# Performance work log

Hardware: AMD Instinct MI355X
Metric: run time of the kernel (lower is better)

## Reference

```python
import jax, jax.numpy as jnp
import numpy as np

BN, C, T = 512, 32, 4096
TARGET = 256


def setup_inputs() -> dict:
    key = jax.random.key(0)
    k1, k2, k3 = jax.random.split(key, 3)
    features = jax.random.normal(k1, (BN, C, T), dtype=jnp.float32)
    mask = jax.random.uniform(k2, (BN, C, T), dtype=jnp.float32)
    valid_lengths = jax.random.randint(k3, (BN,), 0, T, dtype=jnp.int64)
    return {"features": features, "mask": mask,
            "valid_lengths": valid_lengths, "target_len": TARGET}


def _pool(v, si, ei, counts):
    # v: [BN, C, T]; si/ei: [BN, K]; counts: [BN, K]
    bn, c, t = v.shape
    cs = jnp.cumsum(v, axis=-1)
    cs = jnp.concatenate([jnp.zeros((bn, c, 1), cs.dtype), cs], axis=-1)  # [BN,C,T+1]
    s = jnp.take_along_axis(cs, si[:, None, :], axis=-1)  # [BN,C,K] (idx broadcast over C)
    e = jnp.take_along_axis(cs, ei[:, None, :], axis=-1)
    return (e - s) / counts[:, None, :].astype(v.dtype)


def reference(features, mask, valid_lengths, target_len):
    bn, c, t = features.shape
    K = max(int(target_len), 1)
    lengths = jnp.clip(valid_lengths, 1, t)                       # [BN]
    # zero out everything before the trailing valid window
    time_idx = jnp.arange(t, dtype=lengths.dtype)
    rmask = (time_idx[None, :] >= (t - lengths)[:, None]).astype(features.dtype)  # [BN,T]
    f = features * rmask[:, None, :]
    m = mask * rmask[:, None, :]
    # adaptive-pool bin boundaries within the trailing window
    offsets = (t - lengths)[:, None]                              # [BN,1]
    steps = jnp.arange(K + 1, dtype=lengths.dtype)                # [K+1]
    scaled = lengths[:, None] * steps[None, :]                    # [BN,K+1]
    start_rel = scaled[:, :-1] // K
    end_rel = (scaled[:, 1:] + K - 1) // K
    si = jnp.clip(start_rel + offsets, 0, t)
    ei = jnp.clip(end_rel + offsets, 0, t)
    counts = jnp.clip(ei - si, 1, None)                           # [BN,K]
    pooled_feats = _pool(f, si, ei, counts)
    pooled_mask = _pool(m, si, ei, counts)
    return pooled_feats, pooled_mask
```

## Files before the change

### kernel.cpp

```cpp
#include <hip/hip_runtime.h>

#define BN 512
#define CCH 32
#define TT 4096

__device__ __forceinline__ int padidx(int i) { return i + ((i >> 5) << 2); }

__global__ __launch_bounds__(256) void adaptive_pool_lds(
    const float* __restrict__ f, const float* __restrict__ m,
    const int* __restrict__ vlen,
    float* __restrict__ out_f, float* __restrict__ out_m, int K)
{
    __shared__ float sf[4608];
    __shared__ float sm[4608];

    int bc = blockIdx.x;
    int b  = bc / CCH;

    bool is64 = ((vlen[1] | vlen[3] | vlen[5] | vlen[7] |
                  vlen[9] | vlen[11] | vlen[13] | vlen[15]) == 0);
    int len = is64 ? vlen[2 * b] : vlen[b];

    int L = len < 1 ? 1 : (len > TT ? TT : len);
    int off = TT - L;
    int a0 = off & ~3;

    const float* fr = f + (size_t)bc * TT;
    const float* mr = m + (size_t)bc * TT;

    int nv = (TT - a0) >> 2;
    for (int idx = threadIdx.x; idx < nv; idx += 256) {
        int t0 = a0 + (idx << 2);
        float4 vf = *(const float4*)(fr + t0);
        float4 vm = *(const float4*)(mr + t0);
        int p = padidx(t0);
        *(float4*)(&sf[p]) = vf;
        *(float4*)(&sm[p]) = vm;
    }
    __syncthreads();

    for (int k = threadIdx.x; k < K; k += 256) {
        unsigned uL = (unsigned)L, uK = (unsigned)K, uk = (unsigned)k;
        int si = off + (int)((uL * uk) / uK);
        int ei = off + (int)((uL * (uk + 1u) + uK - 1u) / uK);
        if (ei > TT) ei = TT;
        int count = ei - si;
        if (count < 1) count = 1;

        float af = 0.0f, am = 0.0f;
        for (int t = si; t < ei; ++t) {
            int p = padidx(t);
            af += sf[p];
            am += sm[p];
        }
        float inv = 1.0f / (float)count;
        size_t o = (size_t)bc * K + k;
        out_f[o] = af * inv;
        out_m[o] = am * inv;
    }
}

extern "C" void kernel_launch(void* const* d_in, const int* in_sizes, int n_in,
                              void* d_out, int out_size, void* d_ws, size_t ws_size,
                              hipStream_t stream) {
    const float* f    = (const float*)d_in[0];
    const float* m    = (const float*)d_in[1];
    const int*   vlen = (const int*)d_in[2];

    int K = out_size / (2 * BN * CCH);
    if (K < 1) K = 1;

    float* out_f = (float*)d_out;
    float* out_m = out_f + (size_t)BN * CCH * K;

    int grid = BN * CCH;
    adaptive_pool_lds<<<grid, 256, 0, stream>>>(f, m, vlen, out_f, out_m, K);
}
```

Before: 61.60 us.

## Process multiple rows per block with register-prefetched software pipelining

Each block now handles eight (batch,channel) rows in a grid-strided fashion. The global loads for the next row are issued into registers before pooling the current row from LDS, so memory latency overlaps with compute. The grid shrinks eightfold, which cuts block launch overhead but risks tail imbalance across rows with varying valid lengths and higher register pressure.

```diff
diff --git a/kernel.cpp b/kernel.cpp
--- a/kernel.cpp
+++ b/kernel.cpp
@@ -3,10 +3,11 @@
 #define BN 512
 #define CCH 32
 #define TT 4096
+#define RPB 8
 
 __device__ __forceinline__ int padidx(int i) { return i + ((i >> 5) << 2); }
 
-__global__ __launch_bounds__(256) void adaptive_pool_lds(
+__global__ __launch_bounds__(256) void pool_pipe(
     const float* __restrict__ f, const float* __restrict__ m,
     const int* __restrict__ vlen,
     float* __restrict__ out_f, float* __restrict__ out_m, int K)
@@ -14,50 +15,88 @@
     __shared__ float sf[4608];
     __shared__ float sm[4608];
 
-    int bc = blockIdx.x;
-    int b  = bc / CCH;
+    const int tid = threadIdx.x;
+    const int nb  = gridDim.x;
 
     bool is64 = ((vlen[1] | vlen[3] | vlen[5] | vlen[7] |
                   vlen[9] | vlen[11] | vlen[13] | vlen[15]) == 0);
-    int len = is64 ? vlen[2 * b] : vlen[b];
 
-    int L = len < 1 ? 1 : (len > TT ? TT : len);
-    int off = TT - L;
-    int a0 = off & ~3;
+    float4 rf0, rf1, rf2, rf3, rm0, rm1, rm2, rm3;
+    int bc, L, off, a0, nv;
 
-    const float* fr = f + (size_t)bc * TT;
-    const float* mr = m + (size_t)bc * TT;
+    #define ROW_PARAMS(j)                                              \
+        do {                                                           \
+            bc = blockIdx.x + (j) * nb;                                \
+            int b_ = bc / CCH;                                         \
+            int len_ = is64 ? vlen[2 * b_] : vlen[b_];                 \
+            L = len_ < 1 ? 1 : (len_ > TT ? TT : len_);                \
+            off = TT - L;                                              \
+            a0 = off & ~3;                                             \
+            nv = (TT - a0) >> 2;                                       \
+        } while (0)
 
-    int nv = (TT - a0) >> 2;
-    for (int idx = threadIdx.x; idx < nv; idx += 256) {
-        int t0 = a0 + (idx << 2);
-        float4 vf = *(const float4*)(fr + t0);
-        float4 vm = *(const float4*)(mr + t0);
-        int p = padidx(t0);
-        *(float4*)(&sf[p]) = vf;
-        *(float4*)(&sm[p]) = vm;
+    #define ISSUE_LOADS()                                              \
+        do {                                                           \
+            const float* fr_ = f + (size_t)bc * TT + a0;               \
+            const float* mr_ = m + (size_t)bc * TT + a0;               \
+            int i0_ = tid, i1_ = tid + 256, i2_ = tid + 512, i3_ = tid + 768; \
+            if (i0_ < nv) { rf0 = *(const float4*)(fr_ + 4 * i0_);     \
+                            rm0 = *(const float4*)(mr_ + 4 * i0_); }   \
+            if (i1_ < nv) { rf1 = *(const float4*)(fr_ + 4 * i1_);     \
+                            rm1 = *(const float4*)(mr_ + 4 * i1_); }   \
+            if (i2_ < nv) { rf2 = *(const float4*)(fr_ + 4 * i2_);     \
+                            rm2 = *(const float4*)(mr_ + 4 * i2_); }   \
+            if (i3_ < nv) { rf3 = *(const float4*)(fr_ + 4 * i3_);     \
+                            rm3 = *(const float4*)(mr_ + 4 * i3_); }   \
+        } while (0)
+
+    ROW_PARAMS(0);
+    ISSUE_LOADS();
+
+    for (int j = 0; j < RPB; ++j) {
+        {
+            int i0_ = tid, i1_ = tid + 256, i2_ = tid + 512, i3_ = tid + 768;
+            if (i0_ < nv) { int p = padidx(a0 + 4 * i0_);
+                            *(float4*)&sf[p] = rf0; *(float4*)&sm[p] = rm0; }
+            if (i1_ < nv) { int p = padidx(a0 + 4 * i1_);
+                            *(float4*)&sf[p] = rf1; *(float4*)&sm[p] = rm1; }
+            if (i2_ < nv) { int p = padidx(a0 + 4 * i2_);
+                            *(float4*)&sf[p] = rf2; *(float4*)&sm[p] = rm2; }
+            if (i3_ < nv) { int p = padidx(a0 + 4 * i3_);
+                            *(float4*)&sf[p] = rf3; *(float4*)&sm[p] = rm3; }
+        }
+        __syncthreads();
+
+        int cbc = bc, cL = L, coff = off;
+
+        if (j + 1 < RPB) {
+            ROW_PARAMS(j + 1);
+            ISSUE_LOADS();
+        }
+
+        for (int k = tid; k < K; k += 256) {
+            unsigned uL = (unsigned)cL, uK = (unsigned)K, uk = (unsigned)k;
+            int si = coff + (int)((uL * uk) / uK);
+            int ei = coff + (int)((uL * (uk + 1u) + uK - 1u) / uK);
+            if (ei > TT) ei = TT;
+            int count = ei - si;
+            if (count < 1) count = 1;
+
+            float af = 0.0f, am = 0.0f;
+            for (int t = si; t < ei; ++t) {
+                int p = padidx(t);
+                af += sf[p];
+                am += sm[p];
+            }
+            float inv = 1.0f / (float)count;
+            size_t o = (size_t)cbc * K + k;
+            out_f[o] = af * inv;
+            out_m[o] = am * inv;
+        }
+        __syncthreads();
     }
-    __syncthreads();
-
-    for (int k = threadIdx.x; k < K; k += 256) {
-        unsigned uL = (unsigned)L, uK = (unsigned)K, uk = (unsigned)k;
-        int si = off + (int)((uL * uk) / uK);
-        int ei = off + (int)((uL * (uk + 1u) + uK - 1u) / uK);
-        if (ei > TT) ei = TT;
-        int count = ei - si;
-        if (count < 1) count = 1;
-
-        float af = 0.0f, am = 0.0f;
-        for (int t = si; t < ei; ++t) {
-            int p = padidx(t);
-            af += sf[p];
-            am += sm[p];
-        }
-        float inv = 1.0f / (float)count;
-        size_t o = (size_t)bc * K + k;
-        out_f[o] = af * inv;
-        out_m[o] = am * inv;
-    }
+    #undef ROW_PARAMS
+    #undef ISSUE_LOADS
 }
 
 extern "C" void kernel_launch(void* const* d_in, const int* in_sizes, int n_in,
@@ -73,6 +112,6 @@
     float* out_f = (float*)d_out;
     float* out_m = out_f + (size_t)BN * CCH * K;
 
-    int grid = BN * CCH;
-    adaptive_pool_lds<<<grid, 256, 0, stream>>>(f, m, vlen, out_f, out_m, K);
+    int grid = (BN * CCH) / RPB;
+    pool_pipe<<<grid, 256, 0, stream>>>(f, m, vlen, out_f, out_m, K);
 }
```

Measured after the change: 56.23 us (median of 2 runs). -8.7%, faster.

## Split each row into four single-wave blocks over output segments

Applied to the files above, without the earlier changes.

Each (batch, channel) row is now handled by four 64-thread blocks, each covering a quarter of the K outputs. Each block loads only the time range its bins need into a much smaller LDS buffer. This shrinks LDS use per block and raises occupancy. The cost is four times as many blocks, each doing redundant setup and reading vlen.

```diff
diff --git a/kernel.cpp b/kernel.cpp
--- a/kernel.cpp
+++ b/kernel.cpp
@@ -3,53 +3,69 @@
 #define BN 512
 #define CCH 32
 #define TT 4096
+#define SEG 4
 
 __device__ __forceinline__ int padidx(int i) { return i + ((i >> 5) << 2); }
 
-__global__ __launch_bounds__(256) void adaptive_pool_lds(
+#define SLDS 1160
+
+__global__ __launch_bounds__(64) void pool_waveseg(
     const float* __restrict__ f, const float* __restrict__ m,
     const int* __restrict__ vlen,
     float* __restrict__ out_f, float* __restrict__ out_m, int K)
 {
-    __shared__ float sf[4608];
-    __shared__ float sm[4608];
+    __shared__ float sf[SLDS];
+    __shared__ float sm[SLDS];
 
-    int bc = blockIdx.x;
-    int b  = bc / CCH;
+    const int wid  = blockIdx.x;
+    const int seg  = wid & (SEG - 1);
+    const int bc   = wid >> 2;
+    const int b    = bc / CCH;
+    const int lane = threadIdx.x;
 
     bool is64 = ((vlen[1] | vlen[3] | vlen[5] | vlen[7] |
                   vlen[9] | vlen[11] | vlen[13] | vlen[15]) == 0);
     int len = is64 ? vlen[2 * b] : vlen[b];
 
-    int L = len < 1 ? 1 : (len > TT ? TT : len);
+    int L   = len < 1 ? 1 : (len > TT ? TT : len);
     int off = TT - L;
-    int a0 = off & ~3;
+
+    int BK = (K + SEG - 1) / SEG;
+    int k0 = seg * BK;
+    int k1 = k0 + BK; if (k1 > K) k1 = K;
+    if (k0 >= K) return;
+
+    unsigned uL = (unsigned)L, uK = (unsigned)K;
+
+    int ts = off + (int)((uL * (unsigned)k0) / uK);
+    int te = off + (int)((uL * (unsigned)k1 + uK - 1u) / uK);
+    if (te > TT) te = TT;
+    int a0 = ts & ~3;
+    int nv = (te - a0 + 3) >> 2;
 
     const float* fr = f + (size_t)bc * TT;
     const float* mr = m + (size_t)bc * TT;
 
-    int nv = (TT - a0) >> 2;
-    for (int idx = threadIdx.x; idx < nv; idx += 256) {
-        int t0 = a0 + (idx << 2);
+    for (int i = lane; i < nv; i += 64) {
+        int t0 = a0 + (i << 2);
         float4 vf = *(const float4*)(fr + t0);
         float4 vm = *(const float4*)(mr + t0);
-        int p = padidx(t0);
-        *(float4*)(&sf[p]) = vf;
-        *(float4*)(&sm[p]) = vm;
+        int p = padidx(i << 2);
+        *(float4*)&sf[p] = vf;
+        *(float4*)&sm[p] = vm;
     }
     __syncthreads();
 
-    for (int k = threadIdx.x; k < K; k += 256) {
-        unsigned uL = (unsigned)L, uK = (unsigned)K, uk = (unsigned)k;
-        int si = off + (int)((uL * uk) / uK);
-        int ei = off + (int)((uL * (uk + 1u) + uK - 1u) / uK);
+    for (int k = k0 + lane; k < k1; k += 64) {
+        int si = off + (int)((uL * (unsigned)k) / uK);
+        int ei = off + (int)((uL * (unsigned)(k + 1) + uK - 1u) / uK);
         if (ei > TT) ei = TT;
         int count = ei - si;
         if (count < 1) count = 1;
 
         float af = 0.0f, am = 0.0f;
         for (int t = si; t < ei; ++t) {
-            int p = padidx(t);
+            int p = padidx(t - a0);
             af += sf[p];
             am += sm[p];
         }
@@ -73,6 +89,6 @@
     float* out_f = (float*)d_out;
     float* out_m = out_f + (size_t)BN * CCH * K;
 
-    int grid = BN * CCH;
-    adaptive_pool_lds<<<grid, 256, 0, stream>>>(f, m, vlen, out_f, out_m, K);
+    int grid = BN * CCH * SEG;
+    pool_waveseg<<<grid, 64, 0, stream>>>(f, m, vlen, out_f, out_m, K);
 }
```

Measured after the change: 61.49 us. About the same (-0.2%).

## Software-pipeline row loads through registers with single LDS buffer and 4 rows per block

Applied to the files above, without the earlier changes.

Each block now processes four (batch,channel) rows and alternates features and mask through one LDS buffer. The next global load is prefetched into registers while the current buffer is being summed. The goal is to overlap HBM latency with the LDS reduction and to halve LDS use so more blocks fit per CU. It also swaps the integer division for a shift when K is a power of two. The trade-offs are a grid four times smaller and more __syncthreads per row, which may hurt latency hiding across blocks.

```diff
diff --git a/kernel.cpp b/kernel.cpp
--- a/kernel.cpp
+++ b/kernel.cpp
@@ -3,61 +3,104 @@
 #define BN 512
 #define CCH 32
 #define TT 4096
+#define RPB 4
 
 __device__ __forceinline__ int padidx(int i) { return i + ((i >> 5) << 2); }
 
-__global__ __launch_bounds__(256) void adaptive_pool_lds(
+__global__ __launch_bounds__(256) void pool_phased(
     const float* __restrict__ f, const float* __restrict__ m,
     const int* __restrict__ vlen,
-    float* __restrict__ out_f, float* __restrict__ out_m, int K)
+    float* __restrict__ out_f, float* __restrict__ out_m,
+    int K, int kshift)
 {
-    __shared__ float sf[4608];
-    __shared__ float sm[4608];
+    __shared__ float sb[4608];
 
-    int bc = blockIdx.x;
-    int b  = bc / CCH;
+    const int tid = threadIdx.x;
+    const int nb  = gridDim.x;
 
     bool is64 = ((vlen[1] | vlen[3] | vlen[5] | vlen[7] |
                   vlen[9] | vlen[11] | vlen[13] | vlen[15]) == 0);
-    int len = is64 ? vlen[2 * b] : vlen[b];
 
-    int L = len < 1 ? 1 : (len > TT ? TT : len);
-    int off = TT - L;
-    int a0 = off & ~3;
+    float4 r0, r1, r2, r3;
+    int cbc, cL, coff, ca0, cnv;
+    int wa0, wnv;
 
-    const float* fr = f + (size_t)bc * TT;
-    const float* mr = m + (size_t)bc * TT;
+    #define ROWP(J, BC, L_, OFF, A0, NV)                               \
+        do {                                                           \
+            BC = blockIdx.x + (J) * nb;                                \
+            int b_ = (BC) >> 5;                      \
+            int len_ = is64 ? vlen[2 * b_] : vlen[b_];                 \
+            L_ = len_ < 1 ? 1 : (len_ > TT ? TT : len_);               \
+            OFF = TT - L_;                                             \
+            A0 = OFF & ~3;                                             \
+            NV = (TT - A0) >> 2;                                       \
+        } while (0)
 
-    int nv = (TT - a0) >> 2;
-    for (int idx = threadIdx.x; idx < nv; idx += 256) {
-        int t0 = a0 + (idx << 2);
-        float4 vf = *(const float4*)(fr + t0);
-        float4 vm = *(const float4*)(mr + t0);
-        int p = padidx(t0);
-        *(float4*)(&sf[p]) = vf;
-        *(float4*)(&sm[p]) = vm;
+    #define LOADR(SRC, NV)                                             \
+        do {                                                           \
+            int i0_ = tid, i1_ = tid + 256, i2_ = tid + 512, i3_ = tid + 768; \
+            if (i0_ < (NV)) r0 = *(const float4*)((SRC) + 4 * i0_);    \
+            if (i1_ < (NV)) r1 = *(const float4*)((SRC) + 4 * i1_);    \
+            if (i2_ < (NV)) r2 = *(const float4*)((SRC) + 4 * i2_);    \
+            if (i3_ < (NV)) r3 = *(const float4*)((SRC) + 4 * i3_);    \
+        } while (0)
+
+    #define WRITE_LDS()                                                \
+        do {                                                           \
+            int i0_ = tid, i1_ = tid + 256, i2_ = tid + 512, i3_ = tid + 768; \
+            if (i0_ < wnv) { int p = padidx(wa0 + 4 * i0_); *(float4*)&sb[p] = r0; } \
+            if (i1_ < wnv) { int p = padidx(wa0 + 4 * i1_); *(float4*)&sb[p] = r1; } \
+            if (i2_ < wnv) { int p = padidx(wa0 + 4 * i2_); *(float4*)&sb[p] = r2; } \
+            if (i3_ < wnv) { int p = padidx(wa0 + 4 * i3_); *(float4*)&sb[p] = r3; } \
+        } while (0)
+
+    #define COMPUTE(OUTP)                                              \
+        for (int k = tid; k < K; k += 256) {                           \
+            unsigned uL = (unsigned)cL, uK = (unsigned)K, uk = (unsigned)k; \
+            unsigned q0 = uL * uk, q1 = uL * (uk + 1u) + uK - 1u;      \
+            int si, ei;                                                \
+            if (kshift >= 0) { si = coff + (int)(q0 >> kshift);        \
+                               ei = coff + (int)(q1 >> kshift); }      \
+            else             { si = coff + (int)(q0 / uK);             \
+                               ei = coff + (int)(q1 / uK); }           \
+            if (ei > TT) ei = TT;                                      \
+            int count = ei - si; if (count < 1) count = 1;             \
+            float acc = 0.0f;                                          \
+            for (int t = si; t < ei; ++t) acc += sb[padidx(t)];        \
+            (OUTP)[(size_t)cbc * K + k] = acc / (float)count;          \
+        }
+
+    ROWP(0, cbc, cL, coff, ca0, cnv);
+    LOADR(f + (size_t)cbc * TT + ca0, cnv);
+    wa0 = ca0; wnv = cnv;
+
+    for (int j = 0; j < RPB; ++j) {
+        WRITE_LDS();
+        __syncthreads();
+        LOADR(m + (size_t)cbc * TT + ca0, cnv);
+        wa0 = ca0; wnv = cnv;
+        COMPUTE(out_f);
+        __syncthreads();
+
+        WRITE_LDS();
+        __syncthreads();
+        if (j + 1 < RPB) {
+            int nbc, nL, noff, na0, nnv;
+            ROWP(j + 1, nbc, nL, noff, na0, nnv);
+            LOADR(f + (size_t)nbc * TT + na0, nnv);
+            wa0 = na0; wnv = nnv;
+            COMPUTE(out_m);
+            __syncthreads();
+            cbc = nbc; cL = nL; coff = noff; ca0 = na0; cnv = nnv;
+        } else {
+            COMPUTE(out_m);
+            __syncthreads();
+        }
     }
-    __syncthreads();
-
-    for (int k = threadIdx.x; k < K; k += 256) {
-        unsigned uL = (unsigned)L, uK = (unsigned)K, uk = (unsigned)k;
-        int si = off + (int)((uL * uk) / uK);
-        int ei = off + (int)((uL * (uk + 1u) + uK - 1u) / uK);
-        if (ei > TT) ei = TT;
-        int count = ei - si;
-        if (count < 1) count = 1;
-
-        float af = 0.0f, am = 0.0f;
-        for (int t = si; t < ei; ++t) {
-            int p = padidx(t);
-            af += sf[p];
-            am += sm[p];
-        }
-        float inv = 1.0f / (float)count;
-        size_t o = (size_t)bc * K + k;
-        out_f[o] = af * inv;
-        out_m[o] = am * inv;
-    }
+    #undef ROWP
+    #undef LOADR
+    #undef WRITE_LDS
+    #undef COMPUTE
 }
 
 extern "C" void kernel_launch(void* const* d_in, const int* in_sizes, int n_in,
@@ -69,10 +112,11 @@
 
     int K = out_size / (2 * BN * CCH);
     if (K < 1) K = 1;
+    int kshift = ((K & (K - 1)) == 0) ? __builtin_ctz(K) : -1;
 
     float* out_f = (float*)d_out;
     float* out_m = out_f + (size_t)BN * CCH * K;
 
-    int grid = BN * CCH;
-    adaptive_pool_lds<<<grid, 256, 0, stream>>>(f, m, vlen, out_f, out_m, K);
+    int grid = (BN * CCH) / RPB;
+    pool_phased<<<grid, 256, 0, stream>>>(f, m, vlen, out_f, out_m, K, kshift);
 }
```

Result: faster. 56.70 us (-7.9%).
